# Kernel tuning notes

Measured on AMD Instinct MI355X. Metric: run time of the kernel, lower is better.

## Reference

```python
import jax, jax.numpy as jnp
import numpy as np

GRID_RES = (128, 128, 128)
NUM_RAYS = 8192
NUM_COEFFS = 9  # (sh_degree+1)^2, sh_degree=2
NEAR, FAR = 0.1, 3.0
SCENE_MIN, SCENE_MAX = -1.0, 1.0  # default scene_bounds [-1,1]^3


def sh_basis_deg2(dirs):
    """Degree-2 real SH basis, dirs [..., 3] -> [..., 9]. Matches SphericalHarmonics.eval_sh_basis."""
    zero = jnp.sum(dirs * dirs, axis=-1, keepdims=True) < 1e-8
    dirs = jnp.where(zero, jnp.asarray([0.0, 0.0, 1.0], dirs.dtype), dirs)
    dirs = dirs / jnp.linalg.norm(dirs, axis=-1, keepdims=True)
    x, y, z = dirs[..., 0], dirs[..., 1], dirs[..., 2]
    return jnp.stack([
        0.282095 * jnp.ones_like(x),
        0.488603 * y, 0.488603 * z, 0.488603 * x,
        1.092548 * x * y, 1.092548 * y * z,
        0.315392 * (3.0 * z * z - 1.0),
        1.092548 * x * z, 0.546274 * (x * x - y * y),
    ], axis=-1)


def trilerp(grid, pts, has_channels):
    """align_corners=True trilinear interpolation.
    grid: [H,W,D] or [H,W,D,C,K]; pts: [...,3] in [-1,1].
    Returns [...] or [...,C,K].
    """
    dims = jnp.asarray([grid.shape[0] - 1, grid.shape[1] - 1, grid.shape[2] - 1], pts.dtype)
    p = (pts + 1.0) * 0.5 * dims               # voxel-space coords
    f = jnp.floor(p)
    c = jnp.ceil(p)
    frac = p - f
    fi = jnp.clip(f, 0.0, dims).astype(jnp.int32)
    ci = jnp.clip(c, 0.0, dims).astype(jnp.int32)
    out = None
    for dx in (0, 1):
        for dy in (0, 1):
            for dz in (0, 1):
                ix = ci[..., 0] if dx else fi[..., 0]
                iy = ci[..., 1] if dy else fi[..., 1]
                iz = ci[..., 2] if dz else fi[..., 2]
                w = ((frac[..., 0] if dx else 1.0 - frac[..., 0])
                     * (frac[..., 1] if dy else 1.0 - frac[..., 1])
                     * (frac[..., 2] if dz else 1.0 - frac[..., 2]))
                g = grid[ix, iy, iz]           # [...,] or [...,C,K]
                if has_channels:
                    w = w[..., None, None]
                term = w * g
                out = term if out is None else out + term
    return out


def setup_inputs() -> dict:
    key = jax.random.key(0)
    k1, k2, k3, k4 = jax.random.split(key, 4)
    density_grid = jax.random.normal(k1, GRID_RES, dtype=jnp.float32)
    sh_grid = jax.random.normal(k2, (*GRID_RES, 3, NUM_COEFFS), dtype=jnp.float32)
    ray_origins = jax.random.normal(k3, (NUM_RAYS, 3), dtype=jnp.float32)
    ray_directions = jax.random.normal(k4, (NUM_RAYS, 3), dtype=jnp.float32)
    return {
        "density_grid": density_grid,
        "sh_grid": sh_grid,
        "ray_origins": ray_origins,
        "ray_directions": ray_directions,
        "num_samples": 128,
    }


def reference(density_grid, sh_grid, ray_origins, ray_directions, num_samples):
    dtype = ray_origins.dtype
    t = jnp.linspace(NEAR, FAR, num_samples, dtype=dtype)                       # [S]
    pts = ray_origins[:, None, :] + t[None, :, None] * ray_directions[:, None, :]  # [N,S,3]
    norm_pts = 2.0 * (pts - SCENE_MIN) / (SCENE_MAX - SCENE_MIN) - 1.0          # -> [-1,1]

    sigma = trilerp(density_grid, norm_pts, has_channels=False)                 # [N,S]
    sh = trilerp(sh_grid, norm_pts, has_channels=True)                          # [N,S,3,K]

    basis = sh_basis_deg2(ray_directions)                                       # [N,K]
    rgb = jax.nn.sigmoid(jnp.einsum('nsck,nk->nsc', sh, basis))                 # [N,S,3]

    delta = (FAR - NEAR) / (num_samples - 1)
    alpha = 1.0 - jnp.exp(-jax.nn.relu(sigma) * delta)                          # [N,S]
    trans = jnp.cumprod(1.0 - alpha + 1e-10, axis=-1)
    trans = jnp.concatenate([jnp.ones_like(trans[:, :1]), trans[:, :-1]], axis=-1)
    weights = alpha * trans                                                     # [N,S]

    rgb_out = jnp.sum(weights[..., None] * rgb, axis=1)                         # [N,3]
    return rgb_out
```

## Files before the change

### kernel.cpp

```cpp
#include <hip/hip_runtime.h>

static constexpr float NEAR_T = 0.1f;
static constexpr float FAR_T  = 3.0f;

__global__ __launch_bounds__(256)
void plenoxel_render(const float* __restrict__ density,
                     const float* __restrict__ sh,
                     const float* __restrict__ origins,
                     const float* __restrict__ dirs,
                     const int*  __restrict__ ns_ptr,
                     float* __restrict__ out,
                     int nrays)
{
    const int lane = threadIdx.x & 63;
    const int ray  = (int)((blockIdx.x * blockDim.x + threadIdx.x) >> 6);
    if (ray >= nrays) return;

    const int ns = *ns_ptr;
    const float step = (FAR_T - NEAR_T) / (float)(ns - 1);

    const float ox = origins[ray*3+0];
    const float oy = origins[ray*3+1];
    const float oz = origins[ray*3+2];
    const float dx = dirs[ray*3+0];
    const float dy = dirs[ray*3+1];
    const float dz = dirs[ray*3+2];

    float nx = dx, ny = dy, nz = dz;
    float nn = nx*nx + ny*ny + nz*nz;
    if (nn < 1e-8f) { nx = 0.0f; ny = 0.0f; nz = 1.0f; nn = 1.0f; }
    const float inv = 1.0f / sqrtf(nn);
    nx *= inv; ny *= inv; nz *= inv;

    const float B0 = 0.282095f;
    const float B1 = 0.488603f * ny;
    const float B2 = 0.488603f * nz;
    const float B3 = 0.488603f * nx;
    const float B4 = 1.092548f * nx * ny;
    const float B5 = 1.092548f * ny * nz;
    const float B6 = 0.315392f * (3.0f * nz * nz - 1.0f);
    const float B7 = 1.092548f * nx * nz;
    const float B8 = 0.546274f * (nx * nx - ny * ny);

    float alpha2[2];
    float frv[2][3];
    int xb2[2][2], yb2[2][2], zb2[2][2];

    #pragma unroll
    for (int si = 0; si < 2; ++si) {
        const int s = 2*lane + si;
        float sg = 0.0f;
        if (s < ns) {
            const float t = NEAR_T + (float)s * step;
            float px = ox + t*dx;
            float py = oy + t*dy;
            float pz = oz + t*dz;
            px = 2.0f*(px + 1.0f)*0.5f - 1.0f;
            py = 2.0f*(py + 1.0f)*0.5f - 1.0f;
            pz = 2.0f*(pz + 1.0f)*0.5f - 1.0f;
            const float pvx = (px + 1.0f) * 0.5f * 127.0f;
            const float pvy = (py + 1.0f) * 0.5f * 127.0f;
            const float pvz = (pz + 1.0f) * 0.5f * 127.0f;

            const float fx = floorf(pvx), fy = floorf(pvy), fz = floorf(pvz);
            const float frx = pvx - fx, fry = pvy - fy, frz = pvz - fz;
            const int x0 = (int)fminf(fmaxf(fx, 0.0f), 127.0f);
            const int y0 = (int)fminf(fmaxf(fy, 0.0f), 127.0f);
            const int z0 = (int)fminf(fmaxf(fz, 0.0f), 127.0f);
            const int x1 = (int)fminf(fmaxf(ceilf(pvx), 0.0f), 127.0f);
            const int y1 = (int)fminf(fmaxf(ceilf(pvy), 0.0f), 127.0f);
            const int z1 = (int)fminf(fmaxf(ceilf(pvz), 0.0f), 127.0f);

            frv[si][0] = frx; frv[si][1] = fry; frv[si][2] = frz;
            xb2[si][0] = x0 << 14; xb2[si][1] = x1 << 14;
            yb2[si][0] = y0 << 7;  yb2[si][1] = y1 << 7;
            zb2[si][0] = z0;       zb2[si][1] = z1;

            float dv[8];
            #pragma unroll
            for (int cx = 0; cx < 2; ++cx)
                #pragma unroll
                for (int cy = 0; cy < 2; ++cy)
                    #pragma unroll
                    for (int cz = 0; cz < 2; ++cz)
                        dv[cx*4+cy*2+cz] = density[xb2[si][cx] + yb2[si][cy] + zb2[si][cz]];

            const float wx0 = 1.0f - frx, wy0 = 1.0f - fry, wz0 = 1.0f - frz;
            sg  = (wx0*wy0*wz0) * dv[0];
            sg += (wx0*wy0*frz) * dv[1];
            sg += (wx0*fry*wz0) * dv[2];
            sg += (wx0*fry*frz) * dv[3];
            sg += (frx*wy0*wz0) * dv[4];
            sg += (frx*wy0*frz) * dv[5];
            sg += (frx*fry*wz0) * dv[6];
            sg += (frx*fry*frz) * dv[7];

            alpha2[si] = 1.0f - expf(-fmaxf(sg, 0.0f) * step);
        } else {
            alpha2[si] = 0.0f;
            frv[si][0] = frv[si][1] = frv[si][2] = 0.0f;
            xb2[si][0] = xb2[si][1] = 0;
            yb2[si][0] = yb2[si][1] = 0;
            zb2[si][0] = zb2[si][1] = 0;
        }
    }

    const float a0 = (1.0f - alpha2[0]) + 1e-10f;
    const float a1 = (1.0f - alpha2[1]) + 1e-10f;

    float incl = a0 * a1;
    #pragma unroll
    for (int off = 1; off < 64; off <<= 1) {
        const float v = __shfl_up(incl, off, 64);
        incl = (lane >= off) ? incl * v : incl;
    }
    float excl = __shfl_up(incl, 1, 64);
    excl = (lane == 0) ? 1.0f : excl;

    const float wgt0 = alpha2[0] * excl;
    const float wgt1 = alpha2[1] * (excl * a0);
    const float wgt[2] = {wgt0, wgt1};

    float cr = 0.0f, cg = 0.0f, cb = 0.0f;

    #pragma unroll
    for (int si = 0; si < 2; ++si) {
        const float w = wgt[si];
        if (w > 0.0f) {
            const float frx = frv[si][0], fry = frv[si][1], frz = frv[si][2];
            const float wxv[2] = {1.0f - frx, frx};
            const float wyv[2] = {1.0f - fry, fry};
            const float wzv[2] = {1.0f - frz, frz};

            float r0 = 0.0f, r1 = 0.0f, r2 = 0.0f;
            #pragma unroll
            for (int cx = 0; cx < 2; ++cx) {
                #pragma unroll
                for (int cy = 0; cy < 2; ++cy) {
                    #pragma unroll
                    for (int cz = 0; cz < 2; ++cz) {
                        const float cw = wxv[cx] * wyv[cy] * wzv[cz];
                        const int base = xb2[si][cx] + yb2[si][cy] + zb2[si][cz];
                        const float* sp = sh + (long long)base * 27;
                        const float4 L0 = *(const float4*)(sp + 0);
                        const float4 L1 = *(const float4*)(sp + 4);
                        const float4 L2 = *(const float4*)(sp + 8);
                        const float4 L3 = *(const float4*)(sp + 12);
                        const float4 L4 = *(const float4*)(sp + 16);
                        const float4 L5 = *(const float4*)(sp + 20);
                        const float4 L6 = *(const float4*)(sp + 23);

                        const float d0 = L0.x*B0 + L0.y*B1 + L0.z*B2 + L0.w*B3
                                       + L1.x*B4 + L1.y*B5 + L1.z*B6 + L1.w*B7
                                       + L2.x*B8;
                        const float d1 = L2.y*B0 + L2.z*B1 + L2.w*B2
                                       + L3.x*B3 + L3.y*B4 + L3.z*B5 + L3.w*B6
                                       + L4.x*B7 + L4.y*B8;
                        const float d2 = L4.z*B0 + L4.w*B1
                                       + L5.x*B2 + L5.y*B3 + L5.z*B4 + L5.w*B5
                                       + L6.y*B6 + L6.z*B7 + L6.w*B8;

                        r0 = fmaf(cw, d0, r0);
                        r1 = fmaf(cw, d1, r1);
                        r2 = fmaf(cw, d2, r2);
                    }
                }
            }
            cr = fmaf(w, 1.0f / (1.0f + expf(-r0)), cr);
            cg = fmaf(w, 1.0f / (1.0f + expf(-r1)), cg);
            cb = fmaf(w, 1.0f / (1.0f + expf(-r2)), cb);
        }
    }

    #pragma unroll
    for (int off = 32; off; off >>= 1) {
        cr += __shfl_down(cr, off, 64);
        cg += __shfl_down(cg, off, 64);
        cb += __shfl_down(cb, off, 64);
    }

    if (lane == 0) {
        out[ray*3+0] = cr;
        out[ray*3+1] = cg;
        out[ray*3+2] = cb;
    }
}

extern "C" void kernel_launch(void* const* d_in, const int* in_sizes, int n_in,
                              void* d_out, int out_size, void* d_ws, size_t ws_size,
                              hipStream_t stream) {
    const float* density = (const float*)d_in[0];
    const float* sh      = (const float*)d_in[1];
    const float* origins = (const float*)d_in[2];
    const float* dirs    = (const float*)d_in[3];
    const int*   ns_ptr  = (const int*)d_in[4];
    float* out = (float*)d_out;

    const int nrays = in_sizes[2] / 3;
    const int threads = 256;
    const int blocks = (nrays * 64 + threads - 1) / threads;
    plenoxel_render<<<blocks, threads, 0, stream>>>(density, sh, origins, dirs,
                                                    ns_ptr, out, nrays);
}
```

Baseline: 343.6 us.

## Split renderer into weight pass and corner-parallel SH shading pass

Splits the fused kernel in two. The first kernel computes per-sample transmittance weights and writes them to workspace. The second kernel gives each of the eight trilinear corners of a sample its own lane, so the SH gathers spread across more threads, and it merges results with shuffles and atomics. This targets the latency-bound serial loop of eight 27-float gathers per sample, at the cost of a second launch, a workspace round-trip, recomputed ray setup, and atomic adds. The workspace layout assumes at most 128 samples per ray.

```diff
diff --git a/kernel.cpp b/kernel.cpp
--- a/kernel.cpp
+++ b/kernel.cpp
@@ -2,15 +2,16 @@
 
 static constexpr float NEAR_T = 0.1f;
 static constexpr float FAR_T  = 3.0f;
+static constexpr int   MAX_S  = 128;
 
 __global__ __launch_bounds__(256)
-void plenoxel_render(const float* __restrict__ density,
-                     const float* __restrict__ sh,
-                     const float* __restrict__ origins,
-                     const float* __restrict__ dirs,
-                     const int*  __restrict__ ns_ptr,
-                     float* __restrict__ out,
-                     int nrays)
+void k1_weights(const float* __restrict__ density,
+                const float* __restrict__ origins,
+                const float* __restrict__ dirs,
+                const int*  __restrict__ ns_ptr,
+                float* __restrict__ wgt_ws,
+                float* __restrict__ out,
+                int nrays)
 {
     const int lane = threadIdx.x & 63;
     const int ray  = (int)((blockIdx.x * blockDim.x + threadIdx.x) >> 6);
@@ -26,30 +27,11 @@
     const float dy = dirs[ray*3+1];
     const float dz = dirs[ray*3+2];
 
-    float nx = dx, ny = dy, nz = dz;
-    float nn = nx*nx + ny*ny + nz*nz;
-    if (nn < 1e-8f) { nx = 0.0f; ny = 0.0f; nz = 1.0f; nn = 1.0f; }
-    const float inv = 1.0f / sqrtf(nn);
-    nx *= inv; ny *= inv; nz *= inv;
-
-    const float B0 = 0.282095f;
-    const float B1 = 0.488603f * ny;
-    const float B2 = 0.488603f * nz;
-    const float B3 = 0.488603f * nx;
-    const float B4 = 1.092548f * nx * ny;
-    const float B5 = 1.092548f * ny * nz;
-    const float B6 = 0.315392f * (3.0f * nz * nz - 1.0f);
-    const float B7 = 1.092548f * nx * nz;
-    const float B8 = 0.546274f * (nx * nx - ny * ny);
-
     float alpha2[2];
-    float frv[2][3];
-    int xb2[2][2], yb2[2][2], zb2[2][2];
 
     #pragma unroll
     for (int si = 0; si < 2; ++si) {
         const int s = 2*lane + si;
-        float sg = 0.0f;
         if (s < ns) {
             const float t = NEAR_T + (float)s * step;
             float px = ox + t*dx;
@@ -71,10 +53,9 @@
             const int y1 = (int)fminf(fmaxf(ceilf(pvy), 0.0f), 127.0f);
             const int z1 = (int)fminf(fmaxf(ceilf(pvz), 0.0f), 127.0f);
 
-            frv[si][0] = frx; frv[si][1] = fry; frv[si][2] = frz;
-            xb2[si][0] = x0 << 14; xb2[si][1] = x1 << 14;
-            yb2[si][0] = y0 << 7;  yb2[si][1] = y1 << 7;
-            zb2[si][0] = z0;       zb2[si][1] = z1;
+            const int xb[2] = {x0 << 14, x1 << 14};
+            const int yb[2] = {y0 << 7,  y1 << 7};
+            const int zb[2] = {z0, z1};
 
             float dv[8];
             #pragma unroll
@@ -83,9 +64,10 @@
                 for (int cy = 0; cy < 2; ++cy)
                     #pragma unroll
                     for (int cz = 0; cz < 2; ++cz)
-                        dv[cx*4+cy*2+cz] = density[xb2[si][cx] + yb2[si][cy] + zb2[si][cz]];
+                        dv[cx*4+cy*2+cz] = density[xb[cx] + yb[cy] + zb[cz]];
 
             const float wx0 = 1.0f - frx, wy0 = 1.0f - fry, wz0 = 1.0f - frz;
+            float sg;
             sg  = (wx0*wy0*wz0) * dv[0];
             sg += (wx0*wy0*frz) * dv[1];
             sg += (wx0*fry*wz0) * dv[2];
@@ -98,10 +80,6 @@
             alpha2[si] = 1.0f - expf(-fmaxf(sg, 0.0f) * step);
         } else {
             alpha2[si] = 0.0f;
-            frv[si][0] = frv[si][1] = frv[si][2] = 0.0f;
-            xb2[si][0] = xb2[si][1] = 0;
-            yb2[si][0] = yb2[si][1] = 0;
-            zb2[si][0] = zb2[si][1] = 0;
         }
     }
 
@@ -119,70 +97,147 @@
 
     const float wgt0 = alpha2[0] * excl;
     const float wgt1 = alpha2[1] * (excl * a0);
-    const float wgt[2] = {wgt0, wgt1};
-
-    float cr = 0.0f, cg = 0.0f, cb = 0.0f;
-
-    #pragma unroll
-    for (int si = 0; si < 2; ++si) {
-        const float w = wgt[si];
-        if (w > 0.0f) {
-            const float frx = frv[si][0], fry = frv[si][1], frz = frv[si][2];
-            const float wxv[2] = {1.0f - frx, frx};
-            const float wyv[2] = {1.0f - fry, fry};
-            const float wzv[2] = {1.0f - frz, frz};
-
-            float r0 = 0.0f, r1 = 0.0f, r2 = 0.0f;
-            #pragma unroll
-            for (int cx = 0; cx < 2; ++cx) {
-                #pragma unroll
-                for (int cy = 0; cy < 2; ++cy) {
-                    #pragma unroll
-                    for (int cz = 0; cz < 2; ++cz) {
-                        const float cw = wxv[cx] * wyv[cy] * wzv[cz];
-                        const int base = xb2[si][cx] + yb2[si][cy] + zb2[si][cz];
-                        const float* sp = sh + (long long)base * 27;
-                        const float4 L0 = *(const float4*)(sp + 0);
-                        const float4 L1 = *(const float4*)(sp + 4);
-                        const float4 L2 = *(const float4*)(sp + 8);
-                        const float4 L3 = *(const float4*)(sp + 12);
-                        const float4 L4 = *(const float4*)(sp + 16);
-                        const float4 L5 = *(const float4*)(sp + 20);
-                        const float4 L6 = *(const float4*)(sp + 23);
-
-                        const float d0 = L0.x*B0 + L0.y*B1 + L0.z*B2 + L0.w*B3
-                                       + L1.x*B4 + L1.y*B5 + L1.z*B6 + L1.w*B7
-                                       + L2.x*B8;
-                        const float d1 = L2.y*B0 + L2.z*B1 + L2.w*B2
-                                       + L3.x*B3 + L3.y*B4 + L3.z*B5 + L3.w*B6
-                                       + L4.x*B7 + L4.y*B8;
-                        const float d2 = L4.z*B0 + L4.w*B1
-                                       + L5.x*B2 + L5.y*B3 + L5.z*B4 + L5.w*B5
-                                       + L6.y*B6 + L6.z*B7 + L6.w*B8;
-
-                        r0 = fmaf(cw, d0, r0);
-                        r1 = fmaf(cw, d1, r1);
-                        r2 = fmaf(cw, d2, r2);
-                    }
-                }
-            }
-            cr = fmaf(w, 1.0f / (1.0f + expf(-r0)), cr);
-            cg = fmaf(w, 1.0f / (1.0f + expf(-r1)), cg);
-            cb = fmaf(w, 1.0f / (1.0f + expf(-r2)), cb);
-        }
-    }
-
-    #pragma unroll
-    for (int off = 32; off; off >>= 1) {
-        cr += __shfl_down(cr, off, 64);
-        cg += __shfl_down(cg, off, 64);
-        cb += __shfl_down(cb, off, 64);
-    }
+
+    float2* wp = (float2*)(wgt_ws + (long long)ray * MAX_S);
+    wp[lane] = make_float2(wgt0, wgt1);
 
     if (lane == 0) {
-        out[ray*3+0] = cr;
-        out[ray*3+1] = cg;
-        out[ray*3+2] = cb;
+        out[ray*3+0] = 0.0f;
+        out[ray*3+1] = 0.0f;
+        out[ray*3+2] = 0.0f;
+    }
+}
+
+__global__ __launch_bounds__(256)
+void k2_shade(const float* __restrict__ sh,
+              const float* __restrict__ origins,
+              const float* __restrict__ dirs,
+              const int*  __restrict__ ns_ptr,
+              const float* __restrict__ wgt_ws,
+              float* __restrict__ out,
+              int nrays)
+{
+    const int tid    = threadIdx.x;
+    const int wave   = tid >> 6;
+    const int lane   = tid & 63;
+    const int corner = lane & 7;
+    const int sub    = lane >> 3;
+    const int ray    = blockIdx.x >> 2;
+    const int chunk  = blockIdx.x & 3;
+    const int s      = chunk*32 + wave*8 + sub;
+    if (ray >= nrays) return;
+
+    const int ns = *ns_ptr;
+    const float w = (s < ns) ? wgt_ws[(long long)ray * MAX_S + s] : 0.0f;
+
+    float v0 = 0.0f, v1 = 0.0f, v2 = 0.0f;
+
+    if (w > 0.0f) {
+        const float step = (FAR_T - NEAR_T) / (float)(ns - 1);
+
+        const float ox = origins[ray*3+0];
+        const float oy = origins[ray*3+1];
+        const float oz = origins[ray*3+2];
+        const float dx = dirs[ray*3+0];
+        const float dy = dirs[ray*3+1];
+        const float dz = dirs[ray*3+2];
+
+        float nx = dx, ny = dy, nz = dz;
+        float nn = nx*nx + ny*ny + nz*nz;
+        if (nn < 1e-8f) { nx = 0.0f; ny = 0.0f; nz = 1.0f; nn = 1.0f; }
+        const float inv = 1.0f / sqrtf(nn);
+        nx *= inv; ny *= inv; nz *= inv;
+
+        const float B0 = 0.282095f;
+        const float B1 = 0.488603f * ny;
+        const float B2 = 0.488603f * nz;
+        const float B3 = 0.488603f * nx;
+        const float B4 = 1.092548f * nx * ny;
+        const float B5 = 1.092548f * ny * nz;
+        const float B6 = 0.315392f * (3.0f * nz * nz - 1.0f);
+        const float B7 = 1.092548f * nx * nz;
+        const float B8 = 0.546274f * (nx * nx - ny * ny);
+
+        const float t = NEAR_T + (float)s * step;
+        float px = ox + t*dx;
+        float py = oy + t*dy;
+        float pz = oz + t*dz;
+        px = 2.0f*(px + 1.0f)*0.5f - 1.0f;
+        py = 2.0f*(py + 1.0f)*0.5f - 1.0f;
+        pz = 2.0f*(pz + 1.0f)*0.5f - 1.0f;
+        const float pvx = (px + 1.0f) * 0.5f * 127.0f;
+        const float pvy = (py + 1.0f) * 0.5f * 127.0f;
+        const float pvz = (pz + 1.0f) * 0.5f * 127.0f;
+
+        const float fx = floorf(pvx), fy = floorf(pvy), fz = floorf(pvz);
+        const float frx = pvx - fx, fry = pvy - fy, frz = pvz - fz;
+        const int x0 = (int)fminf(fmaxf(fx, 0.0f), 127.0f);
+        const int y0 = (int)fminf(fmaxf(fy, 0.0f), 127.0f);
+        const int z0 = (int)fminf(fmaxf(fz, 0.0f), 127.0f);
+        const int x1 = (int)fminf(fmaxf(ceilf(pvx), 0.0f), 127.0f);
+        const int y1 = (int)fminf(fmaxf(ceilf(pvy), 0.0f), 127.0f);
+        const int z1 = (int)fminf(fmaxf(ceilf(pvz), 0.0f), 127.0f);
+
+        const int cx = (corner >> 2) & 1;
+        const int cy = (corner >> 1) & 1;
+        const int cz = corner & 1;
+
+        const float wx = cx ? frx : (1.0f - frx);
+        const float wy = cy ? fry : (1.0f - fry);
+        const float wz = cz ? frz : (1.0f - frz);
+        const float cw = wx * wy * wz;
+
+        const int base = ((cx ? x1 : x0) << 14) | ((cy ? y1 : y0) << 7) | (cz ? z1 : z0);
+        const float* sp = sh + (long long)base * 27;
+
+        const float4 L0 = *(const float4*)(sp + 0);
+        const float4 L1 = *(const float4*)(sp + 4);
+        const float4 L2 = *(const float4*)(sp + 8);
+        const float4 L3 = *(const float4*)(sp + 12);
+        const float4 L4 = *(const float4*)(sp + 16);
+        const float4 L5 = *(const float4*)(sp + 20);
+        const float4 L6 = *(const float4*)(sp + 23);
+
+        const float d0 = L0.x*B0 + L0.y*B1 + L0.z*B2 + L0.w*B3
+                       + L1.x*B4 + L1.y*B5 + L1.z*B6 + L1.w*B7
+                       + L2.x*B8;
+        const float d1 = L2.y*B0 + L2.z*B1 + L2.w*B2
+                       + L3.x*B3 + L3.y*B4 + L3.z*B5 + L3.w*B6
+                       + L4.x*B7 + L4.y*B8;
+        const float d2 = L4.z*B0 + L4.w*B1
+                       + L5.x*B2 + L5.y*B3 + L5.z*B4 + L5.w*B5
+                       + L6.y*B6 + L6.z*B7 + L6.w*B8;
+
+        v0 = cw * d0;
+        v1 = cw * d1;
+        v2 = cw * d2;
+    }
+
+    #pragma unroll
+    for (int m = 1; m <= 4; m <<= 1) {
+        v0 += __shfl_xor(v0, m, 64);
+        v1 += __shfl_xor(v1, m, 64);
+        v2 += __shfl_xor(v2, m, 64);
+    }
+
+    float c0 = 0.0f, c1 = 0.0f, c2 = 0.0f;
+    if (corner == 0 && w > 0.0f) {
+        c0 = w / (1.0f + expf(-v0));
+        c1 = w / (1.0f + expf(-v1));
+        c2 = w / (1.0f + expf(-v2));
+    }
+
+    #pragma unroll
+    for (int m = 8; m <= 32; m <<= 1) {
+        c0 += __shfl_xor(c0, m, 64);
+        c1 += __shfl_xor(c1, m, 64);
+        c2 += __shfl_xor(c2, m, 64);
+    }
+
+    if (lane == 0) {
+        atomicAdd(&out[ray*3+0], c0);
+        atomicAdd(&out[ray*3+1], c1);
+        atomicAdd(&out[ray*3+2], c2);
     }
 }
 
@@ -195,10 +250,20 @@
     const float* dirs    = (const float*)d_in[3];
     const int*   ns_ptr  = (const int*)d_in[4];
     float* out = (float*)d_out;
+    float* wgt = (float*)d_ws;
 
     const int nrays = in_sizes[2] / 3;
-    const int threads = 256;
-    const int blocks = (nrays * 64 + threads - 1) / threads;
-    plenoxel_render<<<blocks, threads, 0, stream>>>(density, sh, origins, dirs,
-                                                    ns_ptr, out, nrays);
+
+    {
+        const int threads = 256;
+        const int blocks = (nrays * 64 + threads - 1) / threads;
+        k1_weights<<<blocks, threads, 0, stream>>>(density, origins, dirs, ns_ptr,
+                                                   wgt, out, nrays);
+    }
+    {
+        const int threads = 256;
+        const int blocks = nrays * 4;
+        k2_shade<<<blocks, threads, 0, stream>>>(sh, origins, dirs, ns_ptr,
+                                                 wgt, out, nrays);
+    }
 }
```

Measured after the change: 347.8 us. No clear change (+1.2%).
